# Performance work log

Measured on AMD Instinct MI355X. Metric: run time of the kernel, lower is better.

## Reference

```python
import jax, jax.numpy as jnp
import numpy as np

N = 100000
H = 20            # horizon
C = 36            # classes
MV = 200000       # vehicle edges
MO = 400000       # obstacle edges
STEP = 2.0        # TRAJECTORY_PIONTS_LENGTH
DIST_COST = 1.0
OBS_COST = 1.0
OBS_RADIUS = 1.0
VEH_COST = 1.0
VEH_RADIUS = 2.0


def setup_inputs() -> dict:
    key = jax.random.key(0)
    k1, k2, k3, k4, k5, k6 = jax.random.split(key, 6)
    # X: [type, x, y, t_x/r, t_y]; all rows vehicles (type 0) so trajectories are live
    feats = jax.random.normal(k1, (N, 4), dtype=jnp.float32) * 10.0
    X = jnp.concatenate([jnp.zeros((N, 1), jnp.float32), feats], axis=1)
    prediction = jax.random.normal(k2, (N, H * C), dtype=jnp.float32)
    ev0 = jax.random.randint(k3, (MV,), 0, N, dtype=jnp.int32)
    off = jax.random.randint(k4, (MV,), 1, N, dtype=jnp.int32)
    ev1 = (ev0 + off) % N  # guarantee no self-edges
    edges_vehicles = jnp.stack([ev0, ev1], axis=0)
    eo0 = jax.random.randint(k5, (MO,), 0, N, dtype=jnp.int32)
    eo1 = jax.random.randint(k6, (MO,), 0, N, dtype=jnp.int32)
    edges_obstacles = jnp.stack([eo0, eo1], axis=0)
    return {"X": X, "prediction": prediction,
            "edges_vehicles": edges_vehicles, "edges_obstacles": edges_obstacles}


def reference(X, prediction, edges_vehicles, edges_obstacles):
    # class decoding: angle = argmax_class * (2pi/C) * max_logit
    pred = prediction.reshape(-1, H, C)
    max_vals = jnp.max(pred, axis=-1)                      # (N,H)
    max_cls = jnp.argmax(pred, axis=-1).astype(pred.dtype)  # (N,H)
    ang = max_cls * (2.0 * np.pi / C) * max_vals
    vec = jnp.stack([jnp.cos(ang), jnp.sin(ang)], axis=-1)  # (N,H,2)

    vmask = X[:, 0] == 0
    # sequential rollout == cumulative sum of unit steps from initial position
    traj = X[:, None, 1:3] + jnp.cumsum(vec * STEP, axis=1)  # (N,H,2)
    traj = jnp.where(vmask[:, None, None], traj, 0.0)

    # distance to target, mean over vehicle rows x horizon
    d = jnp.linalg.norm(X[:, None, 3:5] - traj, axis=-1)    # (N,H)
    nveh = jnp.sum(vmask).astype(d.dtype)
    distance_loss = jnp.sum(jnp.where(vmask[:, None], d, 0.0)) / (nveh * H) * DIST_COST

    # obstacle term: gather obstacle rows and trajectory rows along edges
    fo = X[edges_obstacles[0]]                               # (MO,5)
    tt = traj[edges_obstacles[1]]                            # (MO,H,2)
    od = jnp.linalg.norm(fo[:, None, 1:3] - tt, axis=-1)     # (MO,H)
    onear = od < fo[:, None, 3] + OBS_RADIUS
    osafe = jnp.where(onear, od, 1.0)
    ocnt = jnp.sum(onear)
    osum = jnp.sum(jnp.where(onear, 1.0 / osafe, 0.0))
    obstacle_loss = jnp.where(ocnt > 0, osum / jnp.maximum(ocnt, 1), 0.0) * OBS_COST

    # vehicle term: all-pairs horizon-step distances per edge
    ft = traj[edges_vehicles[0]]                             # (MV,H,2)
    tt2 = traj[edges_vehicles[1]]                            # (MV,H,2)
    vd = jnp.linalg.norm(ft[:, :, None, :] - tt2[:, None, :, :], axis=-1)  # (MV,H,H)
    vnear = vd < VEH_RADIUS
    vsafe = jnp.where(vnear, vd, 1.0)
    vcnt = jnp.sum(vnear)
    vsum = jnp.sum(jnp.where(vnear, 1.0 / vsafe, 0.0))
    vehicle_loss = jnp.where(vcnt > 0, vsum / jnp.maximum(vcnt, 1), 0.0) * VEH_COST

    total = distance_loss + obstacle_loss + vehicle_loss
    return (total, distance_loss, obstacle_loss, vehicle_loss)
```

## Files before the change

### kernel.cpp

```cpp
#include <hip/hip_runtime.h>
#include <math.h>

#define HORIZON 20
#define NCLASS  36
constexpr float STEP = 2.0f;
constexpr float TWO_PI_OVER_C = 0.17453292519943295f;
constexpr float OBS_RADIUS = 1.0f;

template <int BS>
__device__ __forceinline__ void block_commit(float sum, unsigned cnt,
                                             float* __restrict__ pOut,
                                             unsigned* __restrict__ cOut) {
    __shared__ float    ls[BS / 64];
    __shared__ unsigned lc[BS / 64];
    #pragma unroll
    for (int off = 32; off > 0; off >>= 1) {
        sum += __shfl_down(sum, off, 64);
        cnt += __shfl_down(cnt, off, 64);
    }
    int wid = threadIdx.x >> 6;
    if ((threadIdx.x & 63) == 0) { ls[wid] = sum; lc[wid] = cnt; }
    __syncthreads();
    if (threadIdx.x == 0) {
        float s = 0.0f; unsigned c = 0u;
        #pragma unroll
        for (int w = 0; w < BS / 64; w++) { s += ls[w]; c += lc[w]; }
        pOut[blockIdx.x] = s;
        cOut[blockIdx.x] = c;
    }
}

__global__ void __launch_bounds__(256) angles_kernel(const float* __restrict__ pred,
                                                     float2* __restrict__ steps,
                                                     int total_rows) {
    __shared__ float2 sm[4][576];
    int wave = threadIdx.x >> 6;
    int lane = threadIdx.x & 63;
    int chunk = blockIdx.x * 4 + wave;
    int row0 = chunk * 64;
    int total_f4 = total_rows * 9;
    const float4* p4 = (const float4*)pred;
    #pragma unroll
    for (int q = 0; q < 9; q++) {
        int gl = q * 64 + lane;
        int g = row0 * 9 + gl;
        float4 v;
        if (g < total_f4) v = p4[g];
        else v = make_float4(-INFINITY, -INFINITY, -INFINITY, -INFINITY);
        int j = gl % 9;
        float m = v.x; int ii = 0;
        if (v.y > m) { m = v.y; ii = 1; }
        if (v.z > m) { m = v.z; ii = 2; }
        if (v.w > m) { m = v.w; ii = 3; }
        sm[wave][gl] = make_float2(m, (float)(j * 4 + ii));
    }
    __syncthreads();
    int row = row0 + lane;
    if (row < total_rows) {
        float best = -INFINITY; float bidx = 0.0f;
        #pragma unroll
        for (int j = 0; j < 9; j++) {
            float2 e = sm[wave][lane * 9 + j];
            if (e.x > best) { best = e.x; bidx = e.y; }
        }
        float ang = bidx * TWO_PI_OVER_C * best;
        float s, c;
        sincosf(ang, &s, &c);
        steps[row] = make_float2(STEP * c, STEP * s);
    }
}

__global__ void __launch_bounds__(256) rollout_kernel(const float* __restrict__ X,
                                                      const float2* __restrict__ steps,
                                                      float2* __restrict__ traj,
                                                      float* __restrict__ distP,
                                                      unsigned* __restrict__ distC,
                                                      int n) {
    int i = blockIdx.x * 256 + threadIdx.x;
    float dsum = 0.0f;
    unsigned vehc = 0;
    if (i < n) {
        const float* xr = X + (size_t)i * 5;
        float typ = xr[0];
        float px = xr[1], py = xr[2];
        float tx = xr[3], ty = xr[4];
        bool veh = (typ == 0.0f);
        const float4* sp = (const float4*)(steps + (size_t)i * HORIZON);
        float4 buf[10];
        #pragma unroll
        for (int q = 0; q < 10; q++) buf[q] = sp[q];
        float* f = (float*)buf;
        #pragma unroll
        for (int h = 0; h < HORIZON; h++) {
            px += f[2 * h]; py += f[2 * h + 1];
            float ox = veh ? px : 0.0f;
            float oy = veh ? py : 0.0f;
            f[2 * h] = ox; f[2 * h + 1] = oy;
            float dx = tx - ox, dy = ty - oy;
            dsum += veh ? sqrtf(fmaf(dy, dy, dx * dx)) : 0.0f;
        }
        float4* tp = (float4*)(traj + (size_t)i * HORIZON);
        #pragma unroll
        for (int q = 0; q < 10; q++) tp[q] = buf[q];
        vehc = veh ? 1u : 0u;
    }
    block_commit<256>(dsum, vehc, distP, distC);
}

__global__ void __launch_bounds__(256) obstacle_kernel(const float* __restrict__ X,
                                                       const int* __restrict__ eo,
                                                       const float2* __restrict__ traj,
                                                       float* __restrict__ obsP,
                                                       unsigned* __restrict__ obsC,
                                                       int mo) {
    int e = blockIdx.x * 256 + threadIdx.x;
    float osum = 0.0f; unsigned ocnt = 0;
    if (e < mo) {
        int src = eo[e];
        int dst = eo[mo + e];
        const float* xr = X + (size_t)src * 5;
        float fx = xr[1], fy = xr[2];
        float thr = xr[3] + OBS_RADIUS;
        float thr2 = thr * thr;
        bool tpos = thr > 0.0f;
        const float4* tp = (const float4*)(traj + (size_t)dst * HORIZON);
        float4 buf[10];
        #pragma unroll
        for (int q = 0; q < 10; q++) buf[q] = tp[q];
        const float* f = (const float*)buf;
        #pragma unroll
        for (int h = 0; h < HORIZON; h++) {
            float dx = fx - f[2 * h], dy = fy - f[2 * h + 1];
            float d2 = fmaf(dy, dy, dx * dx);
            bool near = tpos && (d2 < thr2);
            ocnt += near ? 1u : 0u;
            osum += near ? rsqrtf(d2) : 0.0f;
        }
    }
    block_commit<256>(osum, ocnt, obsP, obsC);
}

__global__ void __launch_bounds__(256) vehicle_kernel(const int* __restrict__ ev,
                                                      const float2* __restrict__ traj,
                                                      float* __restrict__ vehP,
                                                      unsigned* __restrict__ vehC,
                                                      int mv) {
    int t = blockIdx.x * 256 + threadIdx.x;
    int e = t >> 1;
    int half = t & 1;
    float vsum = 0.0f; unsigned vcnt = 0;
    if (e < mv) {
        int a = ev[e];
        int b = ev[mv + e];
        const float4* pb = (const float4*)(traj + (size_t)b * HORIZON);
        float4 tb[10];
        #pragma unroll
        for (int q = 0; q < 10; q++) tb[q] = pb[q];
        const float* fb = (const float*)tb;
        const float2* pa = traj + (size_t)a * HORIZON + half * 10;
        for (int i = 0; i < 10; i++) {
            float2 av = pa[i];
            #pragma unroll
            for (int j = 0; j < HORIZON; j++) {
                float dx = av.x - fb[2 * j];
                float dy = av.y - fb[2 * j + 1];
                float d2 = fmaf(dy, dy, dx * dx);
                bool near = d2 < 4.0f;
                vcnt += near ? 1u : 0u;
                vsum += near ? rsqrtf(d2) : 0.0f;
            }
        }
    }
    block_commit<256>(vsum, vcnt, vehP, vehC);
}

__global__ void __launch_bounds__(256) finalize_kernel(
        const float* __restrict__ distP, const unsigned* __restrict__ distC, int nbR,
        const float* __restrict__ obsP,  const unsigned* __restrict__ obsC,  int nbO,
        const float* __restrict__ vehP,  const unsigned* __restrict__ vehC,  int nbV,
        float* __restrict__ out) {
    double s0 = 0, s1 = 0, s2 = 0;
    unsigned long long c0 = 0, c1 = 0, c2 = 0;
    for (int i = threadIdx.x; i < nbR; i += 256) { s0 += (double)distP[i]; c0 += distC[i]; }
    for (int i = threadIdx.x; i < nbO; i += 256) { s1 += (double)obsP[i];  c1 += obsC[i]; }
    for (int i = threadIdx.x; i < nbV; i += 256) { s2 += (double)vehP[i];  c2 += vehC[i]; }
    __shared__ double ds[3][4];
    __shared__ unsigned long long dc[3][4];
    double sv[3] = {s0, s1, s2};
    unsigned long long cv[3] = {c0, c1, c2};
    #pragma unroll
    for (int k = 0; k < 3; k++) {
        double v = sv[k]; unsigned long long cc = cv[k];
        #pragma unroll
        for (int off = 32; off > 0; off >>= 1) {
            v += __shfl_down(v, off, 64);
            cc += __shfl_down(cc, off, 64);
        }
        if ((threadIdx.x & 63) == 0) { ds[k][threadIdx.x >> 6] = v; dc[k][threadIdx.x >> 6] = cc; }
    }
    __syncthreads();
    if (threadIdx.x == 0) {
        double S[3]; unsigned long long C[3];
        #pragma unroll
        for (int k = 0; k < 3; k++) {
            S[k] = ds[k][0] + ds[k][1] + ds[k][2] + ds[k][3];
            C[k] = dc[k][0] + dc[k][1] + dc[k][2] + dc[k][3];
        }
        float dist = (C[0] > 0) ? (float)(S[0] / ((double)C[0] * (double)HORIZON)) : 0.0f;
        float obs  = (C[1] > 0) ? (float)(S[1] / (double)C[1]) : 0.0f;
        float veh  = (C[2] > 0) ? (float)(S[2] / (double)C[2]) : 0.0f;
        out[0] = dist + obs + veh;
        out[1] = dist;
        out[2] = obs;
        out[3] = veh;
    }
}

extern "C" void kernel_launch(void* const* d_in, const int* in_sizes, int n_in,
                              void* d_out, int out_size, void* d_ws, size_t ws_size,
                              hipStream_t stream) {
    const float* X    = (const float*)d_in[0];
    const float* pred = (const float*)d_in[1];
    const int*   ev   = (const int*)d_in[2];
    const int*   eo   = (const int*)d_in[3];
    int n_nodes = in_sizes[0] / 5;
    int mv = in_sizes[2] / 2;
    int mo = in_sizes[3] / 2;

    int total_rows = n_nodes * HORIZON;
    int nChunks = (total_rows + 63) / 64;
    int nbA = (nChunks + 3) / 4;
    int nbR = (n_nodes + 255) / 256;
    int nbO = (mo + 255) / 256;
    int nbV = (2 * mv + 255) / 256;

    char* w = (char*)d_ws;
    float2* steps = (float2*)w;
    size_t off = (size_t)total_rows * sizeof(float2);
    off = (off + 255) & ~(size_t)255;
    float2* traj = (float2*)(w + off);
    off += (size_t)total_rows * sizeof(float2);
    off = (off + 255) & ~(size_t)255;
    float*    distP = (float*)(w + off);    off += (size_t)nbR * 4;
    unsigned* distC = (unsigned*)(w + off); off += (size_t)nbR * 4;
    float*    obsP  = (float*)(w + off);    off += (size_t)nbO * 4;
    unsigned* obsC  = (unsigned*)(w + off); off += (size_t)nbO * 4;
    float*    vehP  = (float*)(w + off);    off += (size_t)nbV * 4;
    unsigned* vehC  = (unsigned*)(w + off); off += (size_t)nbV * 4;
    float* out = (float*)d_out;

    hipLaunchKernelGGL(angles_kernel, dim3(nbA), dim3(256), 0, stream,
                       pred, steps, total_rows);
    hipLaunchKernelGGL(rollout_kernel, dim3(nbR), dim3(256), 0, stream,
                       X, steps, traj, distP, distC, n_nodes);
    hipLaunchKernelGGL(obstacle_kernel, dim3(nbO), dim3(256), 0, stream,
                       X, eo, traj, obsP, obsC, mo);
    hipLaunchKernelGGL(vehicle_kernel, dim3(nbV), dim3(256), 0, stream,
                       ev, traj, vehP, vehC, mv);
    hipLaunchKernelGGL(finalize_kernel, dim3(1), dim3(256), 0, stream,
                       distP, distC, nbR, obsP, obsC, nbO, vehP, vehC, nbV, out);
}
```

Measured before the change: 474.6 us.

## Fuse obstacle and vehicle edge kernels and precompute compact obstacle info

Merges the obstacle and vehicle edge kernels into one launch that splits its grid by block index, so the two phases can run concurrently and one launch is saved. The rollout kernel now writes a packed float4 per node (position and squared threshold), letting obstacle edges do a single aligned gather and skip the trajectory load when the threshold is non-positive. The vehicle path loads its half of trajectory A as vectorized float4 and fully unrolls the inner loop. The angles kernel splits its shared memory into separate max and index arrays to avoid strided float2 accesses. Together these add register pressure and a mixed-workload grid.

```diff
diff --git a/kernel.cpp b/kernel.cpp
--- a/kernel.cpp
+++ b/kernel.cpp
@@ -10,7 +10,8 @@
 template <int BS>
 __device__ __forceinline__ void block_commit(float sum, unsigned cnt,
                                              float* __restrict__ pOut,
-                                             unsigned* __restrict__ cOut) {
+                                             unsigned* __restrict__ cOut,
+                                             int slot) {
     __shared__ float    ls[BS / 64];
     __shared__ unsigned lc[BS / 64];
     #pragma unroll
@@ -25,15 +26,16 @@
         float s = 0.0f; unsigned c = 0u;
         #pragma unroll
         for (int w = 0; w < BS / 64; w++) { s += ls[w]; c += lc[w]; }
-        pOut[blockIdx.x] = s;
-        cOut[blockIdx.x] = c;
+        pOut[slot] = s;
+        cOut[slot] = c;
     }
 }
 
 __global__ void __launch_bounds__(256) angles_kernel(const float* __restrict__ pred,
                                                      float2* __restrict__ steps,
                                                      int total_rows) {
-    __shared__ float2 sm[4][576];
+    __shared__ float smM[4][576];
+    __shared__ float smI[4][576];
     int wave = threadIdx.x >> 6;
     int lane = threadIdx.x & 63;
     int chunk = blockIdx.x * 4 + wave;
@@ -52,7 +54,8 @@
         if (v.y > m) { m = v.y; ii = 1; }
         if (v.z > m) { m = v.z; ii = 2; }
         if (v.w > m) { m = v.w; ii = 3; }
-        sm[wave][gl] = make_float2(m, (float)(j * 4 + ii));
+        smM[wave][gl] = m;
+        smI[wave][gl] = (float)(j * 4 + ii);
     }
     __syncthreads();
     int row = row0 + lane;
@@ -60,8 +63,9 @@
         float best = -INFINITY; float bidx = 0.0f;
         #pragma unroll
         for (int j = 0; j < 9; j++) {
-            float2 e = sm[wave][lane * 9 + j];
-            if (e.x > best) { best = e.x; bidx = e.y; }
+            float m = smM[wave][lane * 9 + j];
+            float id = smI[wave][lane * 9 + j];
+            if (m > best) { best = m; bidx = id; }
         }
         float ang = bidx * TWO_PI_OVER_C * best;
         float s, c;
@@ -73,6 +77,7 @@
 __global__ void __launch_bounds__(256) rollout_kernel(const float* __restrict__ X,
                                                       const float2* __restrict__ steps,
                                                       float2* __restrict__ traj,
+                                                      float4* __restrict__ obsInfo,
                                                       float* __restrict__ distP,
                                                       unsigned* __restrict__ distC,
                                                       int n) {
@@ -84,6 +89,8 @@
         float typ = xr[0];
         float px = xr[1], py = xr[2];
         float tx = xr[3], ty = xr[4];
+        float thr = tx + OBS_RADIUS;
+        obsInfo[i] = make_float4(px, py, (thr > 0.0f) ? thr * thr : -1.0f, 0.0f);
         bool veh = (typ == 0.0f);
         const float4* sp = (const float4*)(steps + (size_t)i * HORIZON);
         float4 buf[10];
@@ -104,74 +111,76 @@
         for (int q = 0; q < 10; q++) tp[q] = buf[q];
         vehc = veh ? 1u : 0u;
     }
-    block_commit<256>(dsum, vehc, distP, distC);
-}
-
-__global__ void __launch_bounds__(256) obstacle_kernel(const float* __restrict__ X,
-                                                       const int* __restrict__ eo,
-                                                       const float2* __restrict__ traj,
-                                                       float* __restrict__ obsP,
-                                                       unsigned* __restrict__ obsC,
-                                                       int mo) {
-    int e = blockIdx.x * 256 + threadIdx.x;
-    float osum = 0.0f; unsigned ocnt = 0;
-    if (e < mo) {
-        int src = eo[e];
-        int dst = eo[mo + e];
-        const float* xr = X + (size_t)src * 5;
-        float fx = xr[1], fy = xr[2];
-        float thr = xr[3] + OBS_RADIUS;
-        float thr2 = thr * thr;
-        bool tpos = thr > 0.0f;
-        const float4* tp = (const float4*)(traj + (size_t)dst * HORIZON);
-        float4 buf[10];
-        #pragma unroll
-        for (int q = 0; q < 10; q++) buf[q] = tp[q];
-        const float* f = (const float*)buf;
-        #pragma unroll
-        for (int h = 0; h < HORIZON; h++) {
-            float dx = fx - f[2 * h], dy = fy - f[2 * h + 1];
-            float d2 = fmaf(dy, dy, dx * dx);
-            bool near = tpos && (d2 < thr2);
-            ocnt += near ? 1u : 0u;
-            osum += near ? rsqrtf(d2) : 0.0f;
-        }
-    }
-    block_commit<256>(osum, ocnt, obsP, obsC);
-}
-
-__global__ void __launch_bounds__(256) vehicle_kernel(const int* __restrict__ ev,
-                                                      const float2* __restrict__ traj,
-                                                      float* __restrict__ vehP,
-                                                      unsigned* __restrict__ vehC,
-                                                      int mv) {
-    int t = blockIdx.x * 256 + threadIdx.x;
-    int e = t >> 1;
-    int half = t & 1;
-    float vsum = 0.0f; unsigned vcnt = 0;
-    if (e < mv) {
-        int a = ev[e];
-        int b = ev[mv + e];
-        const float4* pb = (const float4*)(traj + (size_t)b * HORIZON);
-        float4 tb[10];
-        #pragma unroll
-        for (int q = 0; q < 10; q++) tb[q] = pb[q];
-        const float* fb = (const float*)tb;
-        const float2* pa = traj + (size_t)a * HORIZON + half * 10;
-        for (int i = 0; i < 10; i++) {
-            float2 av = pa[i];
+    block_commit<256>(dsum, vehc, distP, distC, blockIdx.x);
+}
+
+__global__ void __launch_bounds__(256) edges_kernel(const float4* __restrict__ obsInfo,
+                                                    const int* __restrict__ eo, int mo,
+                                                    const int* __restrict__ ev, int mv,
+                                                    const float2* __restrict__ traj,
+                                                    float* __restrict__ obsP,
+                                                    unsigned* __restrict__ obsC,
+                                                    float* __restrict__ vehP,
+                                                    unsigned* __restrict__ vehC,
+                                                    int nbO) {
+    if ((int)blockIdx.x < nbO) {
+        int e = blockIdx.x * 256 + threadIdx.x;
+        float osum = 0.0f; unsigned ocnt = 0;
+        if (e < mo) {
+            int src = eo[e];
+            int dst = eo[mo + e];
+            float4 info = obsInfo[src];
+            if (info.z >= 0.0f) {
+                const float4* tp = (const float4*)(traj + (size_t)dst * HORIZON);
+                float4 buf[10];
+                #pragma unroll
+                for (int q = 0; q < 10; q++) buf[q] = tp[q];
+                const float* f = (const float*)buf;
+                #pragma unroll
+                for (int h = 0; h < HORIZON; h++) {
+                    float dx = info.x - f[2 * h], dy = info.y - f[2 * h + 1];
+                    float d2 = fmaf(dy, dy, dx * dx);
+                    bool near = d2 < info.z;
+                    ocnt += near ? 1u : 0u;
+                    osum += near ? rsqrtf(d2) : 0.0f;
+                }
+            }
+        }
+        block_commit<256>(osum, ocnt, obsP, obsC, blockIdx.x);
+    } else {
+        int t = (blockIdx.x - nbO) * 256 + threadIdx.x;
+        int e = t >> 1;
+        int half = t & 1;
+        float vsum = 0.0f; unsigned vcnt = 0;
+        if (e < mv) {
+            int a = ev[e];
+            int b = ev[mv + e];
+            const float4* pb = (const float4*)(traj + (size_t)b * HORIZON);
+            float4 tb[10];
             #pragma unroll
-            for (int j = 0; j < HORIZON; j++) {
-                float dx = av.x - fb[2 * j];
-                float dy = av.y - fb[2 * j + 1];
-                float d2 = fmaf(dy, dy, dx * dx);
-                bool near = d2 < 4.0f;
-                vcnt += near ? 1u : 0u;
-                vsum += near ? rsqrtf(d2) : 0.0f;
+            for (int q = 0; q < 10; q++) tb[q] = pb[q];
+            const float* fb = (const float*)tb;
+            const float4* pa = (const float4*)(traj + (size_t)a * HORIZON + half * 10);
+            float4 ta[5];
+            #pragma unroll
+            for (int q = 0; q < 5; q++) ta[q] = pa[q];
+            const float* fa = (const float*)ta;
+            #pragma unroll
+            for (int i = 0; i < 10; i++) {
+                float ax = fa[2 * i], ay = fa[2 * i + 1];
+                #pragma unroll
+                for (int j = 0; j < HORIZON; j++) {
+                    float dx = ax - fb[2 * j];
+                    float dy = ay - fb[2 * j + 1];
+                    float d2 = fmaf(dy, dy, dx * dx);
+                    bool near = d2 < 4.0f;
+                    vcnt += near ? 1u : 0u;
+                    vsum += near ? rsqrtf(d2) : 0.0f;
+                }
             }
         }
-    }
-    block_commit<256>(vsum, vcnt, vehP, vehC);
+        block_commit<256>(vsum, vcnt, vehP, vehC, blockIdx.x - nbO);
+    }
 }
 
 __global__ void __launch_bounds__(256) finalize_kernel(
@@ -241,6 +250,8 @@
     float2* traj = (float2*)(w + off);
     off += (size_t)total_rows * sizeof(float2);
     off = (off + 255) & ~(size_t)255;
+    float4* obsInfo = (float4*)(w + off);   off += (size_t)n_nodes * sizeof(float4);
+    off = (off + 255) & ~(size_t)255;
     float*    distP = (float*)(w + off);    off += (size_t)nbR * 4;
     unsigned* distC = (unsigned*)(w + off); off += (size_t)nbR * 4;
     float*    obsP  = (float*)(w + off);    off += (size_t)nbO * 4;
@@ -252,11 +263,9 @@
     hipLaunchKernelGGL(angles_kernel, dim3(nbA), dim3(256), 0, stream,
                        pred, steps, total_rows);
     hipLaunchKernelGGL(rollout_kernel, dim3(nbR), dim3(256), 0, stream,
-                       X, steps, traj, distP, distC, n_nodes);
-    hipLaunchKernelGGL(obstacle_kernel, dim3(nbO), dim3(256), 0, stream,
-                       X, eo, traj, obsP, obsC, mo);
-    hipLaunchKernelGGL(vehicle_kernel, dim3(nbV), dim3(256), 0, stream,
-                       ev, traj, vehP, vehC, mv);
+                       X, steps, traj, obsInfo, distP, distC, n_nodes);
+    hipLaunchKernelGGL(edges_kernel, dim3(nbO + nbV), dim3(256), 0, stream,
+                       obsInfo, eo, mo, ev, mv, traj, obsP, obsC, vehP, vehC, nbO);
     hipLaunchKernelGGL(finalize_kernel, dim3(1), dim3(256), 0, stream,
                        distP, distC, nbR, obsP, obsC, nbO, vehP, vehC, nbV, out);
 }
```

Measured after the change: 452.9 us. 1.05x faster.
